# Kernel tuning notes

Measured on AMD Instinct MI355X. Metric: run time of the kernel, lower is better.

Reference implementation:

```python
import jax, jax.numpy as jnp
import numpy as np
from jax import lax

FS, DW, CIN, COUT, NCLS, BATCH = 128, 8, 64, 256, 2, 512
K1, S1 = FS // 4, FS // 8          # 32, 16
L = FS * DW                        # 1024
T = (L - K1) // S1 + 1             # 63 SNN timesteps
BN_EPS = 1e-5


@jax.custom_vjp
def spike(u):
    """Heaviside spike on (v - threshold); surrogate grad exp(-|u|) (tau_grad=scale_grad=1)."""
    return (u >= 0).astype(u.dtype)

def _spike_fwd(u):
    return (u >= 0).astype(u.dtype), u

def _spike_bwd(u, g):
    return (g * jnp.exp(-jnp.abs(u)),)

spike.defvjp(_spike_fwd, _spike_bwd)


def cuba(x, threshold, current_decay, voltage_decay):
    """CUBA LIF scan. x: [N,C,T] -> binary spikes [N,C,T].
    i[t] = (1-cd)*i[t-1] + x[t]; v[t] = (1-vd)*v[t-1] + i[t]; s = v>=theta; v *= (1-s)."""
    cd, vd = 1.0 - current_decay, 1.0 - voltage_decay
    xs = jnp.moveaxis(x, -1, 0)  # [T,N,C]
    zero = jnp.zeros(x.shape[:-1], x.dtype)

    def step(carry, xt):
        i, v = carry
        i = cd * i + xt
        v = vd * v + i
        s = spike(v - threshold)
        v = v * (1.0 - s)
        return (i, v), s

    _, s = lax.scan(step, (zero, zero), xs)
    return jnp.moveaxis(s, 0, -1)


def conv1d(x, w, b, stride, pad):
    y = lax.conv_general_dilated(x, w, (stride,), [(pad, pad)],
                                 dimension_numbers=('NCH', 'OIH', 'NCH'))
    return y + b[None, :, None]


def bn(x, g, b, m, v):
    scale = g / jnp.sqrt(v + BN_EPS)
    return (x - m[None, :, None]) * scale[None, :, None] + b[None, :, None]


def setup_inputs() -> dict:
    key = jax.random.key(0)
    ks = jax.random.split(key, 12)
    return {
        'x':       jax.random.normal(ks[0], (BATCH, CIN, L), jnp.float32),
        'conv1_w': jax.random.normal(ks[1], (COUT, CIN, K1), jnp.float32) * 0.05,
        'conv1_b': jax.random.normal(ks[2], (COUT,), jnp.float32) * 0.05,
        'bn1_g':   jax.random.uniform(ks[3], (COUT,), jnp.float32, 0.5, 1.5),
        'bn1_b':   jax.random.normal(ks[4], (COUT,), jnp.float32) * 0.1,
        'bn1_m':   jax.random.normal(ks[5], (COUT,), jnp.float32) * 0.1,
        'bn1_v':   jax.random.uniform(ks[6], (COUT,), jnp.float32, 0.5, 1.5),
        'conv2_w': jax.random.normal(ks[7], (COUT, COUT, 3), jnp.float32) * 0.05,
        'conv2_b': jax.random.normal(ks[8], (COUT,), jnp.float32) * 0.05,
        'bn2_g':   jax.random.uniform(ks[9], (COUT,), jnp.float32, 0.5, 1.5),
        'bn2_b':   jax.random.normal(ks[10], (COUT,), jnp.float32) * 0.1,
        'bn2_m':   jax.random.normal(ks[11], (COUT,), jnp.float32) * 0.1,
        'bn2_v':   jax.random.uniform(jax.random.fold_in(key, 100), (COUT,), jnp.float32, 0.5, 1.5),
        'w1':      jax.random.normal(jax.random.fold_in(key, 101), (COUT, COUT), jnp.float32) * 0.1,
        'w2':      jax.random.normal(jax.random.fold_in(key, 102), (NCLS, COUT), jnp.float32) * 0.1,
    }


def reference(x, conv1_w, conv1_b, bn1_g, bn1_b, bn1_m, bn1_v,
              conv2_w, conv2_b, bn2_g, bn2_b, bn2_m, bn2_v, w1, w2):
    # CNN frontend (eval mode: BN uses running stats, dropout is identity)
    z = bn(conv1d(x, conv1_w, conv1_b, S1, 0), bn1_g, bn1_b, bn1_m, bn1_v)   # [N,COUT,T]
    z = bn(conv1d(z, conv2_w, conv2_b, 1, 1), bn2_g, bn2_b, bn2_m, bn2_v)    # [N,COUT,T]
    # CUBA Input encoder block: threshold=0.3, current_decay=0.9, voltage_decay=0.9
    z = cuba(z, 0.3, 0.9, 0.9)
    # CUBA Dense blocks (bias-free synapse per timestep + LIF): threshold=0.1, cd=1, vd=0.1
    z = cuba(jnp.einsum('oc,nct->not', w1, z), 0.1, 1.0, 0.1)
    z = cuba(jnp.einsum('oc,nct->not', w2, z), 0.1, 1.0, 0.1)
    return z  # binary spike trains [N, n_classes, T]
```

## Files before the change

kernel.cpp:

```cpp
#include <hip/hip_runtime.h>
#include <cstdint>
#include <cstddef>


typedef _Float16 half8 __attribute__((ext_vector_type(8)));
typedef float floatx4 __attribute__((ext_vector_type(4)));

__device__ __forceinline__ void split_f32(float v, _Float16& hi, _Float16& lo) {
    _Float16 h = (_Float16)v;
    hi = h;
    lo = (_Float16)((v - (float)h) * 2048.0f);
}

typedef const __attribute__((address_space(1))) unsigned int* gas_ptr;
typedef __attribute__((address_space(3))) unsigned int* las_ptr;
__device__ __forceinline__ void lds_dma16(const void* g, void* l) {
    __builtin_amdgcn_global_load_lds((gas_ptr)g, (las_ptr)l, 16, 0, 0);
}

__global__ __launch_bounds__(256) void prep_kernel(
    const float* __restrict__ c1w, const float* __restrict__ c1b,
    const float* __restrict__ g1,  const float* __restrict__ b1,
    const float* __restrict__ m1,  const float* __restrict__ v1,
    const float* __restrict__ c2w, const float* __restrict__ c2b,
    const float* __restrict__ g2,  const float* __restrict__ b2,
    const float* __restrict__ m2,  const float* __restrict__ v2,
    const float* __restrict__ w1,
    _Float16* __restrict__ w1h, _Float16* __restrict__ w1l,
    _Float16* __restrict__ w2h, _Float16* __restrict__ w2l,
    _Float16* __restrict__ wdh, _Float16* __restrict__ wdl,
    _Float16* __restrict__ z1ph, _Float16* __restrict__ z1pl,
    float* __restrict__ ab1, float* __restrict__ ab2)
{
    const int id = blockIdx.x * 256 + threadIdx.x;
    if (id < 256) {
        float a1 = g1[id] / sqrtf(v1[id] + 1e-5f);
        ab1[id]       = a1;
        ab1[256 + id] = (c1b[id] - m1[id]) * a1 + b1[id];
        float a2 = g2[id] / sqrtf(v2[id] + 1e-5f);
        ab2[id]       = a2;
        ab2[256 + id] = (c2b[id] - m2[id]) * a2 + b2[id];
    }
    {
        short4 zz = {0, 0, 0, 0};
        for (int idx = id; idx < 98304; idx += 65536) {
            const int n = idx / 192;
            const int r = idx - n * 192;
            const int rs = r >> 6;
            const int row = (rs == 0) ? 0 : (63 + rs);
            const int c0 = (r & 63) * 4;
            const size_t off = ((size_t)n * 66 + row) * 256 + c0;
            *(short4*)&z1ph[off] = zz;
            *(short4*)&z1pl[off] = zz;
        }
    }
    split_f32(w1[id], wdh[id], wdl[id]);
    for (int idx = id; idx < 256 * 2048; idx += 65536)
        split_f32(c1w[idx], w1h[idx], w1l[idx]);
    for (int idx = id; idx < 256 * 768; idx += 65536) {
        const int o  = idx / 768;
        const int r  = idx - o * 768;
        const int dt = r >> 8;
        const int c  = r & 255;
        split_f32(c2w[o * 768 + c * 3 + dt], w2h[idx], w2l[idx]);
    }
}

__global__ __launch_bounds__(256, 2) void conv1_mfma(
    const float* __restrict__ x,
    const _Float16* __restrict__ w1h, const _Float16* __restrict__ w1l,
    const float* __restrict__ ab,
    _Float16* __restrict__ z1ph, _Float16* __restrict__ z1pl)
{
    __shared__ _Float16 Ah[4][128][8];
    __shared__ _Float16 Al[4][128][8];
    __shared__ _Float16 Bh[4][128][8];
    __shared__ _Float16 Bl[4][128][8];

    const int tid = threadIdx.x;
    const int bm = blockIdx.x, bn = blockIdx.y;
    const int lr = tid & 127;
    const int h  = tid >> 7;

    const int am = bm * 128 + lr;
    const int an = am / 63, at = am - an * 63;
    const float*    arow  = x   + (size_t)an * 65536 + at * 16 + h * 16;
    const _Float16* bhrow = w1h + (size_t)(bn * 128 + lr) * 2048 + h * 16;
    const _Float16* blrow = w1l + (size_t)(bn * 128 + lr) * 2048 + h * 16;

    const int lane = tid & 63;
    const int wv   = tid >> 6;
    const int mw   = wv & 1, nw = wv >> 1;
    const int quad = lane >> 4;
    const int l15  = lane & 15;

    floatx4 accA[4][4] = {};
    floatx4 accB[4][4] = {};

    for (int it = 0; it < 64; ++it) {
        const float* ap = arow + it * 1024;
        float va[16];
        *(float4*)&va[0]  = *(const float4*)(ap);
        *(float4*)&va[4]  = *(const float4*)(ap + 4);
        *(float4*)&va[8]  = *(const float4*)(ap + 8);
        *(float4*)&va[12] = *(const float4*)(ap + 12);
        int4 bh0 = *(const int4*)(bhrow + it * 32);
        int4 bh1 = *(const int4*)(bhrow + it * 32 + 8);
        int4 bl0 = *(const int4*)(blrow + it * 32);
        int4 bl1 = *(const int4*)(blrow + it * 32 + 8);

        union U { _Float16 hf[8]; int4 v; };
        U c0h, c0l, c1h, c1l;
#pragma unroll
        for (int j = 0; j < 8; ++j) split_f32(va[j],     c0h.hf[j], c0l.hf[j]);
#pragma unroll
        for (int j = 0; j < 8; ++j) split_f32(va[8 + j], c1h.hf[j], c1l.hf[j]);

        __syncthreads();
        *(int4*)&Ah[2*h  ][lr][0] = c0h.v;
        *(int4*)&Ah[2*h+1][lr][0] = c1h.v;
        *(int4*)&Al[2*h  ][lr][0] = c0l.v;
        *(int4*)&Al[2*h+1][lr][0] = c1l.v;
        *(int4*)&Bh[2*h  ][lr][0] = bh0;
        *(int4*)&Bh[2*h+1][lr][0] = bh1;
        *(int4*)&Bl[2*h  ][lr][0] = bl0;
        *(int4*)&Bl[2*h+1][lr][0] = bl1;
        __syncthreads();

        half8 fah[4], fal[4], fbh[4], fbl[4];
#pragma unroll
        for (int t = 0; t < 4; ++t) {
            fah[t] = *(const half8*)&Ah[quad][mw*64 + t*16 + l15][0];
            fal[t] = *(const half8*)&Al[quad][mw*64 + t*16 + l15][0];
            fbh[t] = *(const half8*)&Bh[quad][nw*64 + t*16 + l15][0];
            fbl[t] = *(const half8*)&Bl[quad][nw*64 + t*16 + l15][0];
        }
#pragma unroll
        for (int ti = 0; ti < 4; ++ti)
#pragma unroll
            for (int tj = 0; tj < 4; ++tj) {
                accA[ti][tj] = __builtin_amdgcn_mfma_f32_16x16x32_f16(fah[ti], fbh[tj], accA[ti][tj], 0, 0, 0);
                accB[ti][tj] = __builtin_amdgcn_mfma_f32_16x16x32_f16(fah[ti], fbl[tj], accB[ti][tj], 0, 0, 0);
                accB[ti][tj] = __builtin_amdgcn_mfma_f32_16x16x32_f16(fal[ti], fbh[tj], accB[ti][tj], 0, 0, 0);
            }
    }

#pragma unroll
    for (int tj = 0; tj < 4; ++tj) {
        const int o = bn*128 + nw*64 + tj*16 + l15;
        const float alpha = ab[o], beta = ab[256 + o];
#pragma unroll
        for (int ti = 0; ti < 4; ++ti) {
            const int m0 = bm*128 + mw*64 + ti*16 + quad*4;
#pragma unroll
            for (int r = 0; r < 4; ++r) {
                float c = accA[ti][tj][r] + accB[ti][tj][r] * (1.0f/2048.0f);
                float z = c * alpha + beta;
                _Float16 zh, zl;
                split_f32(z, zh, zl);
                const int m  = m0 + r;
                const int a2 = m / 63;
                const int t2 = m - a2 * 63;
                const size_t off = ((size_t)a2 * 66 + t2 + 1) * 256 + o;
                z1ph[off] = zh;
                z1pl[off] = zl;
            }
        }
    }
}

__global__ __launch_bounds__(256, 2) void conv2_cuba_mfma(
    const _Float16* __restrict__ z1ph, const _Float16* __restrict__ z1pl,
    const _Float16* __restrict__ w2h, const _Float16* __restrict__ w2l,
    const float* __restrict__ ab, _Float16* __restrict__ s1)
{
    __shared__ _Float16 SMEM[32768];
    _Float16 (*Ah)[128][8] = reinterpret_cast<_Float16(*)[128][8]>(SMEM);
    _Float16 (*Al)[128][8] = reinterpret_cast<_Float16(*)[128][8]>(SMEM + 8192);
    _Float16 (*Bh)[128][8] = reinterpret_cast<_Float16(*)[128][8]>(SMEM + 16384);
    _Float16 (*Bl)[128][8] = reinterpret_cast<_Float16(*)[128][8]>(SMEM + 24576);

    const int tid = threadIdx.x;
    const int bm = blockIdx.x, bn = blockIdx.y;
    const int lr = tid & 127;
    const int h  = tid >> 7;

    const int n0 = bm * 2;
    const int an = lr >> 6, at = lr & 63;
    const _Float16* pAh = z1ph + ((size_t)(n0 + an) * 66 + at) * 256 + h * 8;
    const _Float16* pAl = z1pl + ((size_t)(n0 + an) * 66 + at) * 256 + h * 8;
    const _Float16* pBh = w2h + (size_t)(bn * 128 + lr) * 768 + h * 8;
    const _Float16* pBl = w2l + (size_t)(bn * 128 + lr) * 768 + h * 8;

    const int lane = tid & 63;
    const int wv   = tid >> 6;
    const int mw   = wv & 1, nw = wv >> 1;
    const int quad = lane >> 4;
    const int l15  = lane & 15;

    floatx4 accA[4][4] = {};
    floatx4 accB[4][4] = {};

    for (int it = 0; it < 12; ++it) {
        __syncthreads();
#pragma unroll
        for (int q = 0; q < 4; ++q) {
            lds_dma16(pAh + q * 16, &Ah[q*2 + h][lr][0]);
            lds_dma16(pAl + q * 16, &Al[q*2 + h][lr][0]);
            lds_dma16(pBh + q * 16, &Bh[q*2 + h][lr][0]);
            lds_dma16(pBl + q * 16, &Bl[q*2 + h][lr][0]);
        }
        __syncthreads();

#pragma unroll
        for (int ks = 0; ks < 2; ++ks) {
            half8 fah[4], fal[4], fbh[4], fbl[4];
#pragma unroll
            for (int t = 0; t < 4; ++t) {
                fah[t] = *(const half8*)&Ah[ks*4 + quad][mw*64 + t*16 + l15][0];
                fal[t] = *(const half8*)&Al[ks*4 + quad][mw*64 + t*16 + l15][0];
                fbh[t] = *(const half8*)&Bh[ks*4 + quad][nw*64 + t*16 + l15][0];
                fbl[t] = *(const half8*)&Bl[ks*4 + quad][nw*64 + t*16 + l15][0];
            }
#pragma unroll
            for (int ti = 0; ti < 4; ++ti)
#pragma unroll
                for (int tj = 0; tj < 4; ++tj) {
                    accA[ti][tj] = __builtin_amdgcn_mfma_f32_16x16x32_f16(fah[ti], fbh[tj], accA[ti][tj], 0, 0, 0);
                    accB[ti][tj] = __builtin_amdgcn_mfma_f32_16x16x32_f16(fah[ti], fbl[tj], accB[ti][tj], 0, 0, 0);
                    accB[ti][tj] = __builtin_amdgcn_mfma_f32_16x16x32_f16(fal[ti], fbh[tj], accB[ti][tj], 0, 0, 0);
                }
        }
        pAh += 64; pAl += 64; pBh += 64; pBl += 64;
    }

    __syncthreads();
    float* zt = (float*)SMEM;
#pragma unroll
    for (int tj = 0; tj < 4; ++tj) {
        const int cl = nw*64 + tj*16 + l15;
        const int o  = bn*128 + cl;
        const float alpha = ab[o], beta = ab[256 + o];
#pragma unroll
        for (int ti = 0; ti < 4; ++ti) {
            const int m0 = mw*64 + ti*16 + quad*4;
#pragma unroll
            for (int r = 0; r < 4; ++r) {
                float c = accA[ti][tj][r] + accB[ti][tj][r] * (1.0f/2048.0f);
                zt[(m0 + r) * 128 + cl] = c * alpha + beta;
            }
        }
    }
    __syncthreads();

    const int nl   = tid >> 7;
    const int cloc = tid & 127;
    const int n    = n0 + nl;
    _Float16* srow = s1 + (size_t)n * 16128 + bn*128 + cloc;
    float cur = 0.f, vol = 0.f;
    for (int t = 0; t < 63; ++t) {
        float xv = zt[(nl*64 + t) * 128 + cloc];
        cur = 0.1f * cur + xv;
        vol = 0.1f * vol + cur;
        bool sp = (vol - 0.3f) >= 0.f;
        srow[(size_t)t * 256] = sp ? (_Float16)1.0f : (_Float16)0.0f;
        if (sp) vol = 0.f;
    }
}

__global__ __launch_bounds__(256, 2) void dense1_mask_mfma(
    const _Float16* __restrict__ s1,
    const _Float16* __restrict__ wdh, const _Float16* __restrict__ wdl,
    unsigned long long* __restrict__ M2g)
{
    __shared__ _Float16 SMEM[32768];
    _Float16 (*As)[128][8] = reinterpret_cast<_Float16(*)[128][8]>(SMEM);
    _Float16 (*Bh)[128][8] = reinterpret_cast<_Float16(*)[128][8]>(SMEM + 8192);
    _Float16 (*Bl)[128][8] = reinterpret_cast<_Float16(*)[128][8]>(SMEM + 16384);

    const int tid = threadIdx.x;
    const int bm = blockIdx.x, bn = blockIdx.y;
    const int lr = tid & 127;
    const int h  = tid >> 7;

    const int n0 = bm * 2;
    const int an = lr >> 6, at = lr & 63;
    const _Float16* pA  = s1  + ((size_t)(n0 + an) * 63 + at) * 256 + h * 8;
    const _Float16* pBh = wdh + (size_t)(bn * 128 + lr) * 256 + h * 8;
    const _Float16* pBl = wdl + (size_t)(bn * 128 + lr) * 256 + h * 8;

    const int lane = tid & 63;
    const int wv   = tid >> 6;
    const int mw   = wv & 1, nw = wv >> 1;
    const int quad = lane >> 4;
    const int l15  = lane & 15;

    floatx4 accA[4][4] = {};
    floatx4 accB[4][4] = {};

    for (int it = 0; it < 4; ++it) {
        __syncthreads();
#pragma unroll
        for (int q = 0; q < 4; ++q) {
            lds_dma16(pA  + q * 16, &As[q*2 + h][lr][0]);
            lds_dma16(pBh + q * 16, &Bh[q*2 + h][lr][0]);
            lds_dma16(pBl + q * 16, &Bl[q*2 + h][lr][0]);
        }
        __syncthreads();

#pragma unroll
        for (int ks = 0; ks < 2; ++ks) {
            half8 fa[4], fbh[4], fbl[4];
#pragma unroll
            for (int t = 0; t < 4; ++t) {
                fa[t]  = *(const half8*)&As[ks*4 + quad][mw*64 + t*16 + l15][0];
                fbh[t] = *(const half8*)&Bh[ks*4 + quad][nw*64 + t*16 + l15][0];
                fbl[t] = *(const half8*)&Bl[ks*4 + quad][nw*64 + t*16 + l15][0];
            }
#pragma unroll
            for (int ti = 0; ti < 4; ++ti)
#pragma unroll
                for (int tj = 0; tj < 4; ++tj) {
                    accA[ti][tj] = __builtin_amdgcn_mfma_f32_16x16x32_f16(fa[ti], fbh[tj], accA[ti][tj], 0, 0, 0);
                    accB[ti][tj] = __builtin_amdgcn_mfma_f32_16x16x32_f16(fa[ti], fbl[tj], accB[ti][tj], 0, 0, 0);
                }
        }
        pA += 64; pBh += 64; pBl += 64;
    }

    __syncthreads();
    float* yt = (float*)SMEM;
#pragma unroll
    for (int tj = 0; tj < 4; ++tj) {
        const int cl = nw*64 + tj*16 + l15;
#pragma unroll
        for (int ti = 0; ti < 4; ++ti) {
            const int m0 = mw*64 + ti*16 + quad*4;
#pragma unroll
            for (int r = 0; r < 4; ++r)
                yt[(m0 + r) * 128 + cl] =
                    accA[ti][tj][r] + accB[ti][tj][r] * (1.0f/2048.0f);
        }
    }
    __syncthreads();

    const int nl   = tid >> 7;
    const int oloc = tid & 127;
    unsigned long long mask = 0ull;
    float v = 0.f;
    for (int t = 0; t < 63; ++t) {
        float yv = yt[(nl*64 + t) * 128 + oloc];
        v = 0.9f * v + yv;
        if ((v - 0.1f) >= 0.f) { mask |= (1ull << t); v = 0.f; }
    }
    M2g[(size_t)(n0 + nl) * 256 + bn*128 + oloc] = mask;
}

__global__ __launch_bounds__(256) void snn_tail(
    const unsigned long long* __restrict__ M2g, const float* __restrict__ w2,
    float* __restrict__ out)
{
    __shared__ unsigned long long M2[256];
    __shared__ float Y[2 * 63];
    const int n   = blockIdx.x;
    const int tid = threadIdx.x;

    M2[tid] = M2g[(size_t)n * 256 + tid];
    __syncthreads();

    if (tid < 126) {
        const int cls = tid / 63;
        const int t   = tid - cls * 63;
        const float* wrow = w2 + cls * 256;
        float acc = 0.f;
#pragma unroll 4
        for (int o = 0; o < 256; ++o)
            acc += ((M2[o] >> t) & 1ull) ? wrow[o] : 0.f;
        Y[cls * 63 + t] = acc;
    }
    __syncthreads();
    if (tid < 2) {
        float v = 0.f;
        float* orow = out + (size_t)n * 126 + tid * 63;
        for (int t = 0; t < 63; ++t) {
            v = 0.9f * v + Y[tid * 63 + t];
            float u = v - 0.1f;
            float s = (u >= 0.f) ? 1.f : 0.f;
            orow[t] = s;
            v = (u >= 0.f) ? 0.f : v;
        }
    }
}

extern "C" void kernel_launch(void* const* d_in, const int* in_sizes, int n_in,
                              void* d_out, int out_size, void* d_ws, size_t ws_size,
                              hipStream_t stream)
{
    const float* x    = (const float*)d_in[0];
    const float* c1w  = (const float*)d_in[1];
    const float* c1b  = (const float*)d_in[2];
    const float* g1   = (const float*)d_in[3];
    const float* b1   = (const float*)d_in[4];
    const float* m1   = (const float*)d_in[5];
    const float* v1   = (const float*)d_in[6];
    const float* c2w  = (const float*)d_in[7];
    const float* c2b  = (const float*)d_in[8];
    const float* g2   = (const float*)d_in[9];
    const float* b2   = (const float*)d_in[10];
    const float* m2   = (const float*)d_in[11];
    const float* v2   = (const float*)d_in[12];
    const float* w1   = (const float*)d_in[13];
    const float* w2   = (const float*)d_in[14];
    float* out = (float*)d_out;

    float* ws = (float*)d_ws;
    _Float16* z1ph = (_Float16*)ws;
    _Float16* z1pl = (_Float16*)(ws + 4325376);
    _Float16* s1   = (_Float16*)(ws + 8650752);
    unsigned long long* M2g = (unsigned long long*)(ws + 12779520);
    float*    wsp  = ws + 13041664;
    _Float16* w1h = (_Float16*)wsp;
    _Float16* w1l = (_Float16*)(wsp + 262144);
    _Float16* w2h = (_Float16*)(wsp + 2*262144);
    _Float16* w2l = (_Float16*)(wsp + 2*262144 + 98304);
    _Float16* wdh = (_Float16*)(wsp + 2*262144 + 2*98304);
    _Float16* wdl = (_Float16*)(wsp + 2*262144 + 2*98304 + 32768);
    float*    ab1 = wsp + 2*262144 + 2*98304 + 2*32768;
    float*    ab2 = ab1 + 512;

    prep_kernel<<<256, 256, 0, stream>>>(c1w, c1b, g1, b1, m1, v1,
                                         c2w, c2b, g2, b2, m2, v2,
                                         w1, w1h, w1l, w2h, w2l, wdh, wdl,
                                         z1ph, z1pl, ab1, ab2);
    conv1_mfma<<<dim3(252, 2), 256, 0, stream>>>(x, w1h, w1l, ab1, z1ph, z1pl);
    conv2_cuba_mfma<<<dim3(256, 2), 256, 0, stream>>>(z1ph, z1pl, w2h, w2l, ab2, s1);
    dense1_mask_mfma<<<dim3(256, 2), 256, 0, stream>>>(s1, wdh, wdl, M2g);
    snn_tail<<<512, 256, 0, stream>>>(M2g, w2, out);
}
```

Measured before the change: 429.8 us.

## Fuse conv2+CUBA, dense1+CUBA and output tail into one per-sample kernel

Merges the conv2/CUBA, dense1/CUBA mask and snn_tail kernels into a single kernel where each block handles one sample across all 256 channels. Intermediate spikes stay in a swizzled LDS tile and the LIF scans run straight from MFMA accumulators using lane shuffles, so the s1 and M2 global round trips and two launches go away. In exchange, the full weight matrices are streamed once per sample instead of per half-tile, and the A tile is loaded through registers rather than LDS DMA. The larger LDS footprint and register-resident scans may lower occupancy.

```diff
diff --git a/kernel.cpp b/kernel.cpp
--- a/kernel.cpp
+++ b/kernel.cpp
@@ -169,209 +169,175 @@
     }
 }
 
-__global__ __launch_bounds__(256, 2) void conv2_cuba_mfma(
+__global__ __launch_bounds__(256, 2) void fused_tail(
     const _Float16* __restrict__ z1ph, const _Float16* __restrict__ z1pl,
     const _Float16* __restrict__ w2h, const _Float16* __restrict__ w2l,
-    const float* __restrict__ ab, _Float16* __restrict__ s1)
+    const _Float16* __restrict__ wdh, const _Float16* __restrict__ wdl,
+    const float* __restrict__ ab, const float* __restrict__ w2f,
+    float* __restrict__ out)
 {
-    __shared__ _Float16 SMEM[32768];
-    _Float16 (*Ah)[128][8] = reinterpret_cast<_Float16(*)[128][8]>(SMEM);
-    _Float16 (*Al)[128][8] = reinterpret_cast<_Float16(*)[128][8]>(SMEM + 8192);
-    _Float16 (*Bh)[128][8] = reinterpret_cast<_Float16(*)[128][8]>(SMEM + 16384);
-    _Float16 (*Bl)[128][8] = reinterpret_cast<_Float16(*)[128][8]>(SMEM + 24576);
-
-    const int tid = threadIdx.x;
-    const int bm = blockIdx.x, bn = blockIdx.y;
-    const int lr = tid & 127;
-    const int h  = tid >> 7;
-
-    const int n0 = bm * 2;
-    const int an = lr >> 6, at = lr & 63;
-    const _Float16* pAh = z1ph + ((size_t)(n0 + an) * 66 + at) * 256 + h * 8;
-    const _Float16* pAl = z1pl + ((size_t)(n0 + an) * 66 + at) * 256 + h * 8;
-    const _Float16* pBh = w2h + (size_t)(bn * 128 + lr) * 768 + h * 8;
-    const _Float16* pBl = w2l + (size_t)(bn * 128 + lr) * 768 + h * 8;
-
+    __shared__ _Float16 BSTh[4][256][8];
+    __shared__ _Float16 BSTl[4][256][8];
+    __shared__ _Float16 ASTh[4][64][8];
+    __shared__ _Float16 ASTl[4][64][8];
+    __shared__ _Float16 S1T[64 * 256];
+    __shared__ unsigned long long M2[256];
+    __shared__ float Y[126];
+
+    const int tid  = threadIdx.x;
+    const int n    = blockIdx.x;
     const int lane = tid & 63;
     const int wv   = tid >> 6;
-    const int mw   = wv & 1, nw = wv >> 1;
     const int quad = lane >> 4;
     const int l15  = lane & 15;
+    const int arow = tid & 63;
+    const int kq   = tid >> 6;
+
+    const _Float16* z1h_n = z1ph + (size_t)n * 16896;
+    const _Float16* z1l_n = z1pl + (size_t)n * 16896;
+    const _Float16* w2h_t = w2h + (size_t)tid * 768;
+    const _Float16* w2l_t = w2l + (size_t)tid * 768;
+    const _Float16* wdh_t = wdh + (size_t)tid * 256;
+    const _Float16* wdl_t = wdl + (size_t)tid * 256;
 
     floatx4 accA[4][4] = {};
     floatx4 accB[4][4] = {};
 
-    for (int it = 0; it < 12; ++it) {
-        __syncthreads();
+    S1T[63 * 256 + tid] = (_Float16)0.0f;
+
+    for (int it = 0; it < 24; ++it) {
+        const int dt = it >> 3;
+        const int c0 = (it & 7) * 32;
+        __syncthreads();
+        int4 vh = *(const int4*)(z1h_n + (arow + dt) * 256 + c0 + kq * 8);
+        int4 vl = *(const int4*)(z1l_n + (arow + dt) * 256 + c0 + kq * 8);
 #pragma unroll
         for (int q = 0; q < 4; ++q) {
-            lds_dma16(pAh + q * 16, &Ah[q*2 + h][lr][0]);
-            lds_dma16(pAl + q * 16, &Al[q*2 + h][lr][0]);
-            lds_dma16(pBh + q * 16, &Bh[q*2 + h][lr][0]);
-            lds_dma16(pBl + q * 16, &Bl[q*2 + h][lr][0]);
-        }
-        __syncthreads();
-
-#pragma unroll
-        for (int ks = 0; ks < 2; ++ks) {
-            half8 fah[4], fal[4], fbh[4], fbl[4];
-#pragma unroll
-            for (int t = 0; t < 4; ++t) {
-                fah[t] = *(const half8*)&Ah[ks*4 + quad][mw*64 + t*16 + l15][0];
-                fal[t] = *(const half8*)&Al[ks*4 + quad][mw*64 + t*16 + l15][0];
-                fbh[t] = *(const half8*)&Bh[ks*4 + quad][nw*64 + t*16 + l15][0];
-                fbl[t] = *(const half8*)&Bl[ks*4 + quad][nw*64 + t*16 + l15][0];
-            }
-#pragma unroll
-            for (int ti = 0; ti < 4; ++ti)
-#pragma unroll
-                for (int tj = 0; tj < 4; ++tj) {
-                    accA[ti][tj] = __builtin_amdgcn_mfma_f32_16x16x32_f16(fah[ti], fbh[tj], accA[ti][tj], 0, 0, 0);
-                    accB[ti][tj] = __builtin_amdgcn_mfma_f32_16x16x32_f16(fah[ti], fbl[tj], accB[ti][tj], 0, 0, 0);
-                    accB[ti][tj] = __builtin_amdgcn_mfma_f32_16x16x32_f16(fal[ti], fbh[tj], accB[ti][tj], 0, 0, 0);
+            lds_dma16(w2h_t + it * 32 + q * 8, &BSTh[q][tid][0]);
+            lds_dma16(w2l_t + it * 32 + q * 8, &BSTl[q][tid][0]);
+        }
+        *(int4*)&ASTh[kq][arow][0] = vh;
+        *(int4*)&ASTl[kq][arow][0] = vl;
+        __syncthreads();
+
+        half8 fah[4], fal[4], fbh[4], fbl[4];
+#pragma unroll
+        for (int t = 0; t < 4; ++t) {
+            fah[t] = *(const half8*)&ASTh[quad][t*16 + l15][0];
+            fal[t] = *(const half8*)&ASTl[quad][t*16 + l15][0];
+            fbh[t] = *(const half8*)&BSTh[quad][wv*64 + t*16 + l15][0];
+            fbl[t] = *(const half8*)&BSTl[quad][wv*64 + t*16 + l15][0];
+        }
+#pragma unroll
+        for (int ti = 0; ti < 4; ++ti)
+#pragma unroll
+            for (int tj = 0; tj < 4; ++tj) {
+                accA[ti][tj] = __builtin_amdgcn_mfma_f32_16x16x32_f16(fah[ti], fbh[tj], accA[ti][tj], 0, 0, 0);
+                accB[ti][tj] = __builtin_amdgcn_mfma_f32_16x16x32_f16(fah[ti], fbl[tj], accB[ti][tj], 0, 0, 0);
+                accB[ti][tj] = __builtin_amdgcn_mfma_f32_16x16x32_f16(fal[ti], fbh[tj], accB[ti][tj], 0, 0, 0);
+            }
+    }
+
+    {
+        float al4[4], be4[4], cur[4] = {0,0,0,0}, vol[4] = {0,0,0,0};
+#pragma unroll
+        for (int tj = 0; tj < 4; ++tj) {
+            const int o = wv*64 + tj*16 + l15;
+            al4[tj] = ab[o]; be4[tj] = ab[256 + o];
+        }
+#pragma unroll
+        for (int seg = 0; seg < 16; ++seg) {
+            const int sq = seg & 3, ti = seg >> 2;
+#pragma unroll
+            for (int r = 0; r < 4; ++r) {
+                const int t = seg * 4 + r;
+                if (t < 63) {
+#pragma unroll
+                    for (int tj = 0; tj < 4; ++tj) {
+                        float zown = accA[ti][tj][r] + accB[ti][tj][r] * (1.0f/2048.0f);
+                        float zb = __shfl(zown, l15 + (sq << 4));
+                        float xv = zb * al4[tj] + be4[tj];
+                        cur[tj] = 0.1f * cur[tj] + xv;
+                        vol[tj] = 0.1f * vol[tj] + cur[tj];
+                        bool sp = (vol[tj] - 0.3f) >= 0.f;
+                        if (quad == 0) {
+                            const int o = wv*64 + tj*16 + l15;
+                            S1T[t * 256 + (o ^ ((t & 7) << 3))] =
+                                sp ? (_Float16)1.0f : (_Float16)0.0f;
+                        }
+                        if (sp) vol[tj] = 0.f;
+                    }
                 }
-        }
-        pAh += 64; pAl += 64; pBh += 64; pBl += 64;
-    }
-
-    __syncthreads();
-    float* zt = (float*)SMEM;
-#pragma unroll
-    for (int tj = 0; tj < 4; ++tj) {
-        const int cl = nw*64 + tj*16 + l15;
-        const int o  = bn*128 + cl;
-        const float alpha = ab[o], beta = ab[256 + o];
-#pragma unroll
-        for (int ti = 0; ti < 4; ++ti) {
-            const int m0 = mw*64 + ti*16 + quad*4;
+            }
+        }
+    }
+
+    {
+        const floatx4 zv = {0.f, 0.f, 0.f, 0.f};
+#pragma unroll
+        for (int ti = 0; ti < 4; ++ti)
+#pragma unroll
+            for (int tj = 0; tj < 4; ++tj) { accA[ti][tj] = zv; accB[ti][tj] = zv; }
+    }
+    for (int it = 0; it < 8; ++it) {
+        const int c0 = it * 32;
+        __syncthreads();
+#pragma unroll
+        for (int q = 0; q < 4; ++q) {
+            lds_dma16(wdh_t + c0 + q * 8, &BSTh[q][tid][0]);
+            lds_dma16(wdl_t + c0 + q * 8, &BSTl[q][tid][0]);
+        }
+        __syncthreads();
+
+        half8 fa[4], fbh[4], fbl[4];
+#pragma unroll
+        for (int t = 0; t < 4; ++t) {
+            const int row = t*16 + l15;
+            fa[t] = *(const half8*)&S1T[row * 256 + ((c0 + quad*8) ^ ((row & 7) << 3))];
+            fbh[t] = *(const half8*)&BSTh[quad][wv*64 + t*16 + l15][0];
+            fbl[t] = *(const half8*)&BSTl[quad][wv*64 + t*16 + l15][0];
+        }
+#pragma unroll
+        for (int ti = 0; ti < 4; ++ti)
+#pragma unroll
+            for (int tj = 0; tj < 4; ++tj) {
+                accA[ti][tj] = __builtin_amdgcn_mfma_f32_16x16x32_f16(fa[ti], fbh[tj], accA[ti][tj], 0, 0, 0);
+                accB[ti][tj] = __builtin_amdgcn_mfma_f32_16x16x32_f16(fa[ti], fbl[tj], accB[ti][tj], 0, 0, 0);
+            }
+    }
+
+    {
+        unsigned long long mk[4] = {0ull, 0ull, 0ull, 0ull};
+        float v4[4] = {0.f, 0.f, 0.f, 0.f};
+#pragma unroll
+        for (int seg = 0; seg < 16; ++seg) {
+            const int sq = seg & 3, ti = seg >> 2;
 #pragma unroll
             for (int r = 0; r < 4; ++r) {
-                float c = accA[ti][tj][r] + accB[ti][tj][r] * (1.0f/2048.0f);
-                zt[(m0 + r) * 128 + cl] = c * alpha + beta;
-            }
-        }
-    }
-    __syncthreads();
-
-    const int nl   = tid >> 7;
-    const int cloc = tid & 127;
-    const int n    = n0 + nl;
-    _Float16* srow = s1 + (size_t)n * 16128 + bn*128 + cloc;
-    float cur = 0.f, vol = 0.f;
-    for (int t = 0; t < 63; ++t) {
-        float xv = zt[(nl*64 + t) * 128 + cloc];
-        cur = 0.1f * cur + xv;
-        vol = 0.1f * vol + cur;
-        bool sp = (vol - 0.3f) >= 0.f;
-        srow[(size_t)t * 256] = sp ? (_Float16)1.0f : (_Float16)0.0f;
-        if (sp) vol = 0.f;
-    }
-}
-
-__global__ __launch_bounds__(256, 2) void dense1_mask_mfma(
-    const _Float16* __restrict__ s1,
-    const _Float16* __restrict__ wdh, const _Float16* __restrict__ wdl,
-    unsigned long long* __restrict__ M2g)
-{
-    __shared__ _Float16 SMEM[32768];
-    _Float16 (*As)[128][8] = reinterpret_cast<_Float16(*)[128][8]>(SMEM);
-    _Float16 (*Bh)[128][8] = reinterpret_cast<_Float16(*)[128][8]>(SMEM + 8192);
-    _Float16 (*Bl)[128][8] = reinterpret_cast<_Float16(*)[128][8]>(SMEM + 16384);
-
-    const int tid = threadIdx.x;
-    const int bm = blockIdx.x, bn = blockIdx.y;
-    const int lr = tid & 127;
-    const int h  = tid >> 7;
-
-    const int n0 = bm * 2;
-    const int an = lr >> 6, at = lr & 63;
-    const _Float16* pA  = s1  + ((size_t)(n0 + an) * 63 + at) * 256 + h * 8;
-    const _Float16* pBh = wdh + (size_t)(bn * 128 + lr) * 256 + h * 8;
-    const _Float16* pBl = wdl + (size_t)(bn * 128 + lr) * 256 + h * 8;
-
-    const int lane = tid & 63;
-    const int wv   = tid >> 6;
-    const int mw   = wv & 1, nw = wv >> 1;
-    const int quad = lane >> 4;
-    const int l15  = lane & 15;
-
-    floatx4 accA[4][4] = {};
-    floatx4 accB[4][4] = {};
-
-    for (int it = 0; it < 4; ++it) {
-        __syncthreads();
-#pragma unroll
-        for (int q = 0; q < 4; ++q) {
-            lds_dma16(pA  + q * 16, &As[q*2 + h][lr][0]);
-            lds_dma16(pBh + q * 16, &Bh[q*2 + h][lr][0]);
-            lds_dma16(pBl + q * 16, &Bl[q*2 + h][lr][0]);
-        }
-        __syncthreads();
-
-#pragma unroll
-        for (int ks = 0; ks < 2; ++ks) {
-            half8 fa[4], fbh[4], fbl[4];
-#pragma unroll
-            for (int t = 0; t < 4; ++t) {
-                fa[t]  = *(const half8*)&As[ks*4 + quad][mw*64 + t*16 + l15][0];
-                fbh[t] = *(const half8*)&Bh[ks*4 + quad][nw*64 + t*16 + l15][0];
-                fbl[t] = *(const half8*)&Bl[ks*4 + quad][nw*64 + t*16 + l15][0];
-            }
-#pragma unroll
-            for (int ti = 0; ti < 4; ++ti)
-#pragma unroll
-                for (int tj = 0; tj < 4; ++tj) {
-                    accA[ti][tj] = __builtin_amdgcn_mfma_f32_16x16x32_f16(fa[ti], fbh[tj], accA[ti][tj], 0, 0, 0);
-                    accB[ti][tj] = __builtin_amdgcn_mfma_f32_16x16x32_f16(fa[ti], fbl[tj], accB[ti][tj], 0, 0, 0);
+                const int t = seg * 4 + r;
+                if (t < 63) {
+#pragma unroll
+                    for (int tj = 0; tj < 4; ++tj) {
+                        float yown = accA[ti][tj][r] + accB[ti][tj][r] * (1.0f/2048.0f);
+                        float yb = __shfl(yown, l15 + (sq << 4));
+                        v4[tj] = 0.9f * v4[tj] + yb;
+                        if ((v4[tj] - 0.1f) >= 0.f) { mk[tj] |= (1ull << t); v4[tj] = 0.f; }
+                    }
                 }
-        }
-        pA += 64; pBh += 64; pBl += 64;
-    }
-
-    __syncthreads();
-    float* yt = (float*)SMEM;
-#pragma unroll
-    for (int tj = 0; tj < 4; ++tj) {
-        const int cl = nw*64 + tj*16 + l15;
-#pragma unroll
-        for (int ti = 0; ti < 4; ++ti) {
-            const int m0 = mw*64 + ti*16 + quad*4;
-#pragma unroll
-            for (int r = 0; r < 4; ++r)
-                yt[(m0 + r) * 128 + cl] =
-                    accA[ti][tj][r] + accB[ti][tj][r] * (1.0f/2048.0f);
-        }
-    }
-    __syncthreads();
-
-    const int nl   = tid >> 7;
-    const int oloc = tid & 127;
-    unsigned long long mask = 0ull;
-    float v = 0.f;
-    for (int t = 0; t < 63; ++t) {
-        float yv = yt[(nl*64 + t) * 128 + oloc];
-        v = 0.9f * v + yv;
-        if ((v - 0.1f) >= 0.f) { mask |= (1ull << t); v = 0.f; }
-    }
-    M2g[(size_t)(n0 + nl) * 256 + bn*128 + oloc] = mask;
-}
-
-__global__ __launch_bounds__(256) void snn_tail(
-    const unsigned long long* __restrict__ M2g, const float* __restrict__ w2,
-    float* __restrict__ out)
-{
-    __shared__ unsigned long long M2[256];
-    __shared__ float Y[2 * 63];
-    const int n   = blockIdx.x;
-    const int tid = threadIdx.x;
-
-    M2[tid] = M2g[(size_t)n * 256 + tid];
+            }
+        }
+        if (quad == 0) {
+#pragma unroll
+            for (int tj = 0; tj < 4; ++tj)
+                M2[wv*64 + tj*16 + l15] = mk[tj];
+        }
+    }
     __syncthreads();
 
     if (tid < 126) {
         const int cls = tid / 63;
         const int t   = tid - cls * 63;
-        const float* wrow = w2 + cls * 256;
+        const float* wrow = w2f + cls * 256;
         float acc = 0.f;
 #pragma unroll 4
         for (int o = 0; o < 256; ++o)
@@ -416,9 +382,7 @@
     float* ws = (float*)d_ws;
     _Float16* z1ph = (_Float16*)ws;
     _Float16* z1pl = (_Float16*)(ws + 4325376);
-    _Float16* s1   = (_Float16*)(ws + 8650752);
-    unsigned long long* M2g = (unsigned long long*)(ws + 12779520);
-    float*    wsp  = ws + 13041664;
+    float*    wsp  = ws + 8650752;
     _Float16* w1h = (_Float16*)wsp;
     _Float16* w1l = (_Float16*)(wsp + 262144);
     _Float16* w2h = (_Float16*)(wsp + 2*262144);
@@ -433,7 +397,6 @@
                                          w1, w1h, w1l, w2h, w2l, wdh, wdl,
                                          z1ph, z1pl, ab1, ab2);
     conv1_mfma<<<dim3(252, 2), 256, 0, stream>>>(x, w1h, w1l, ab1, z1ph, z1pl);
-    conv2_cuba_mfma<<<dim3(256, 2), 256, 0, stream>>>(z1ph, z1pl, w2h, w2l, ab2, s1);
-    dense1_mask_mfma<<<dim3(256, 2), 256, 0, stream>>>(s1, wdh, wdl, M2g);
-    snn_tail<<<512, 256, 0, stream>>>(M2g, w2, out);
-}
+    fused_tail<<<512, 256, 0, stream>>>(z1ph, z1pl, w2h, w2l, wdh, wdl,
+                                        ab2, w2, out);
+}
```

Measured after the change: 514.3 us. +19.7%, slower.
